# Optimization experiments

Hardware: AMD Instinct MI355X
Metric: run time of the kernel (lower is better)

The kernel has to match this reference:

```python
import jax, jax.numpy as jnp
import numpy as np

N_NODES = 100000
N_EDGES = 3200000
D_FEAT = 128
N_CLASSES = 8


def setup_inputs() -> dict:
    key = jax.random.key(0)
    ks = jax.random.split(key, 8)
    x = jax.random.normal(ks[0], (N_NODES, D_FEAT), dtype=jnp.float32)
    edge_index = jax.random.randint(ks[1], (2, N_EDGES), 0, N_NODES, dtype=jnp.int64)
    W1 = jax.random.normal(ks[2], (D_FEAT, 32), dtype=jnp.float32) / np.sqrt(D_FEAT)
    b1 = jnp.zeros((32,), dtype=jnp.float32)
    W2 = jax.random.normal(ks[3], (32, 16), dtype=jnp.float32) / np.sqrt(32)
    b2 = jnp.zeros((16,), dtype=jnp.float32)
    Wc = jax.random.normal(ks[4], (16, N_CLASSES), dtype=jnp.float32) / np.sqrt(16)
    bc = jnp.zeros((N_CLASSES,), dtype=jnp.float32)
    return {"x": x, "edge_index": edge_index, "W1": W1, "b1": b1,
            "W2": W2, "b2": b2, "Wc": Wc, "bc": bc}


def _gcn_conv(h, src, dst, norm, W, b, num_nodes):
    # PyG GCNConv: linear transform, then sym-normalized scatter-add, then bias
    h = h @ W                                   # [N, out]
    msg = h[src] * norm[:, None]                # [E+N, out] gather + scale
    out = jax.ops.segment_sum(msg, dst, num_segments=num_nodes)
    return out + b


def reference(x, edge_index, W1, b1, W2, b2, Wc, bc):
    num_nodes = x.shape[0]
    loop = jnp.arange(num_nodes, dtype=edge_index.dtype)
    src = jnp.concatenate([edge_index[0], loop])  # add self-loops (PyG default)
    dst = jnp.concatenate([edge_index[1], loop])
    deg = jax.ops.segment_sum(jnp.ones_like(dst, dtype=x.dtype), dst,
                              num_segments=num_nodes)
    dinv = jnp.where(deg > 0, jax.lax.rsqrt(deg), 0.0)
    norm = dinv[src] * dinv[dst]                # symmetric normalization per edge

    h = _gcn_conv(x, src, dst, norm, W1, b1, num_nodes)
    h = jax.nn.relu(h)
    # dropout p=0.5 is identity in eval mode (training=False)
    h = _gcn_conv(h, src, dst, norm, W2, b2, num_nodes)
    h = jax.nn.relu(h)
    logits = h @ Wc + bc
    return jax.nn.log_softmax(logits, axis=1)
```

## Files before the change

### kernel.cpp

```cpp
#include <hip/hip_runtime.h>
#include <math.h>

#define N_NODES 100000
#define N_EDGES 3200000
#define D_FEAT 128
#define H1 32
#define H2 16
#define NC 8

#define NBUCK 391
#define BCAP 12288
#define HCAP 6144
#define EPB 4096
#define EPT 8

#define P_NODES 32
#define P_CAP 3072

typedef short s16x8 __attribute__((ext_vector_type(8)));
typedef float f32x4 __attribute__((ext_vector_type(4)));

__device__ inline unsigned short f2bf(float f) {
    unsigned int u = __float_as_uint(f);
    u += 0x7FFF + ((u >> 16) & 1);
    return (unsigned short)(u >> 16);
}
__device__ inline float bf2f(unsigned short h) {
    return __uint_as_float((unsigned int)h << 16);
}

__device__ inline int wave_scan_incl(int v, int lane) {
#pragma unroll
    for (int off = 1; off < 64; off <<= 1) {
        const int t = __shfl_up(v, off, 64);
        if (lane >= off) v += t;
    }
    return v;
}


__global__ __launch_bounds__(512) void k_bscatter(const int* __restrict__ ei,
                                                  const float* __restrict__ W1,
                                                  int* __restrict__ bucket_cursor,
                                                  unsigned short* __restrict__ W1f,
                                                  int* __restrict__ ebuf) {
    __shared__ int hist[NBUCK];
    __shared__ int lofs[NBUCK];
    __shared__ int rank[NBUCK];
    __shared__ int gb[NBUCK];
    __shared__ int wsum[8];
    __shared__ int s_is64;
    __shared__ int pay[EPB];
    __shared__ unsigned short pbk[EPB];
    const int tid = threadIdx.x;
    const int lane = tid & 63;
    const int wid = tid >> 6;
    for (int i = tid; i < NBUCK; i += 512) { hist[i] = 0; rank[i] = 0; }
    if (tid < 64) {
        int v = ei[2 * tid + 1];
#pragma unroll
        for (int off = 1; off < 64; off <<= 1) v |= __shfl_xor(v, off, 64);
        if (tid == 0) s_is64 = (v == 0) ? 1 : 0;
    }
    if (blockIdx.x == 0) {
        for (int idx = tid; idx < 2 * 4 * 64 * 8; idx += 512) {
            const int j    = idx & 7;
            const int ln   = (idx >> 3) & 63;
            const int kk   = (idx >> 9) & 3;
            const int nt   = idx >> 11;
            const int k = kk * 32 + ((ln >> 4) << 3) + j;
            const int n = nt * 16 + (ln & 15);
            W1f[idx] = f2bf(W1[k * H1 + n]);
        }
    }
    __syncthreads();
    const int e0 = blockIdx.x * EPB;
    const int n = min(EPB, N_EDGES - e0);
    const bool is64 = (s_is64 != 0);
    int rs[EPT], rd[EPT];
    if (is64) {
#pragma unroll
        for (int k = 0; k < EPT / 2; ++k) {
            const int i = 2 * (tid + k * 512);
            if (i < n) {
                const int e = e0 + i;
                const int4 s = *(const int4*)&ei[2 * e];
                const int4 d = *(const int4*)&ei[2 * N_EDGES + 2 * e];
                rs[2 * k] = s.x; rs[2 * k + 1] = s.z;
                rd[2 * k] = d.x; rd[2 * k + 1] = d.z;
                atomicAdd(&hist[d.x >> 8], 1);
                atomicAdd(&hist[d.z >> 8], 1);
            }
        }
    } else {
#pragma unroll
        for (int k = 0; k < EPT / 2; ++k) {
            const int i = 2 * (tid + k * 512);
            if (i < n) {
                const int e = e0 + i;
                const int2 s = *(const int2*)&ei[e];
                const int2 d = *(const int2*)&ei[N_EDGES + e];
                rs[2 * k] = s.x; rs[2 * k + 1] = s.y;
                rd[2 * k] = d.x; rd[2 * k + 1] = d.y;
                atomicAdd(&hist[d.x >> 8], 1);
                atomicAdd(&hist[d.y >> 8], 1);
            }
        }
    }
    __syncthreads();
    const int own = (tid < NBUCK) ? hist[tid] : 0;
    int incl = wave_scan_incl(own, lane);
    if (lane == 63) wsum[wid] = incl;
    __syncthreads();
    if (tid == 0) {
        int r = 0;
#pragma unroll
        for (int w = 0; w < 8; ++w) { const int t = wsum[w]; wsum[w] = r; r += t; }
    }
    __syncthreads();
    incl += wsum[wid];
    if (tid < NBUCK) {
        lofs[tid] = incl - own;
        if (own > 0) gb[tid] = tid * BCAP + atomicAdd(&bucket_cursor[tid], own);
    }
    __syncthreads();
#pragma unroll
    for (int k = 0; k < EPT / 2; ++k) {
        const int i = 2 * (tid + k * 512);
        if (i < n) {
#pragma unroll
            for (int j = 0; j < 2; ++j) {
                const int b = rd[2 * k + j] >> 8;
                const int p = lofs[b] + atomicAdd(&rank[b], 1);
                pay[p] = (rs[2 * k + j] << 8) | (rd[2 * k + j] & 255);
                pbk[p] = (unsigned short)b;
            }
        }
    }
    __syncthreads();
    for (int p = tid; p < n; p += 512) {
        const int b = pbk[p];
        ebuf[gb[b] + (p - lofs[b])] = pay[p];
    }
}


__global__ __launch_bounds__(512) void k_deg(const int* __restrict__ ebuf,
                                             const int* __restrict__ bucket_cursor,
                                             float* __restrict__ dinv) {
    __shared__ int cnt[256];
    const int b = blockIdx.x;
    const int tid = threadIdx.x;
    if (tid < 256) cnt[tid] = 0;
    __syncthreads();
    const int nb = bucket_cursor[b];
    const int rb = b * BCAP;
    for (int i = tid; i < nb; i += 512)
        atomicAdd(&cnt[ebuf[rb + i] & 255], 1);
    __syncthreads();
    if (tid < 256) {
        const int v = (b << 8) + tid;
        if (v < N_NODES) dinv[v] = rsqrtf(1.0f + (float)cnt[tid]);
    }
}


__global__ __launch_bounds__(256) void k_gemm1m(const float* __restrict__ x,
                                                const unsigned short* __restrict__ W1f,
                                                const float* __restrict__ dinv,
                                                unsigned int* __restrict__ u1q) {
    __shared__ float os[4][16][33];
    const int tid = threadIdx.x;
    const int w = tid >> 6;
    const int lane = tid & 63;
    const int row0 = (blockIdx.x * 4 + w) * 16;
    const bool act = (row0 < N_NODES);
    if (act) {
        const int m = lane & 15;
        const int quad = lane >> 4;
        const s16x8* bf = (const s16x8*)W1f;
        f32x4 acc0 = {0.f, 0.f, 0.f, 0.f};
        f32x4 acc1 = {0.f, 0.f, 0.f, 0.f};
#pragma unroll
        for (int kk = 0; kk < 4; ++kk) {
            const float* xp = x + (size_t)(row0 + m) * D_FEAT + kk * 32 + quad * 8;
            const float4 p0 = ((const float4*)xp)[0];
            const float4 p1 = ((const float4*)xp)[1];
            s16x8 a;
            a[0] = (short)f2bf(p0.x); a[1] = (short)f2bf(p0.y);
            a[2] = (short)f2bf(p0.z); a[3] = (short)f2bf(p0.w);
            a[4] = (short)f2bf(p1.x); a[5] = (short)f2bf(p1.y);
            a[6] = (short)f2bf(p1.z); a[7] = (short)f2bf(p1.w);
            acc0 = __builtin_amdgcn_mfma_f32_16x16x32_bf16(a, bf[kk * 64 + lane], acc0, 0, 0, 0);
            acc1 = __builtin_amdgcn_mfma_f32_16x16x32_bf16(a, bf[(4 + kk) * 64 + lane], acc1, 0, 0, 0);
        }
#pragma unroll
        for (int r = 0; r < 4; ++r) {
            os[w][quad * 4 + r][m]      = acc0[r];
            os[w][quad * 4 + r][16 + m] = acc1[r];
        }
    }
    __syncthreads();
    if (act) {
        const int rl = lane >> 2;
        const int seg = lane & 3;
        const int row = row0 + rl;
        const float dv = dinv[row];
        const float* p = &os[w][rl][seg * 8];
        unsigned int pk0 = __builtin_amdgcn_cvt_pk_fp8_f32(p[0] * dv, p[1] * dv, 0u, false);
        pk0 = __builtin_amdgcn_cvt_pk_fp8_f32(p[2] * dv, p[3] * dv, pk0, true);
        unsigned int pk1 = __builtin_amdgcn_cvt_pk_fp8_f32(p[4] * dv, p[5] * dv, 0u, false);
        pk1 = __builtin_amdgcn_cvt_pk_fp8_f32(p[6] * dv, p[7] * dv, pk1, true);
        uint2 o; o.x = pk0; o.y = pk1;
        ((uint2*)u1q)[(size_t)row * 4 + seg] = o;
    }
}


#define ACC8(Q) do { \
    a0 += __builtin_amdgcn_cvt_f32_fp8((Q).x, 0); \
    a1 += __builtin_amdgcn_cvt_f32_fp8((Q).x, 1); \
    a2 += __builtin_amdgcn_cvt_f32_fp8((Q).x, 2); \
    a3 += __builtin_amdgcn_cvt_f32_fp8((Q).x, 3); \
    a4 += __builtin_amdgcn_cvt_f32_fp8((Q).y, 0); \
    a5 += __builtin_amdgcn_cvt_f32_fp8((Q).y, 1); \
    a6 += __builtin_amdgcn_cvt_f32_fp8((Q).y, 2); \
    a7 += __builtin_amdgcn_cvt_f32_fp8((Q).y, 3); \
} while (0)

__global__ __launch_bounds__(512) void k_fuse1(const int* __restrict__ ebuf,
                                               const int* __restrict__ bucket_cursor,
                                               const unsigned int* __restrict__ u1q,
                                               const float* __restrict__ b1,
                                               const float* __restrict__ W2,
                                               int* __restrict__ row_ptr,
                                               int* __restrict__ col_idx,
                                               unsigned int* __restrict__ u2b) {
    __shared__ int srt[HCAP];
    __shared__ int cnt[256];
    __shared__ int cur[256];
    __shared__ int wsum[8];
    __shared__ int wsum2[4];
    __shared__ float Ws[H1 * H2];
    __shared__ float hs[128][33];
    __shared__ int s_wb, s_base, s_nh;
    const int b = blockIdx.x >> 1;
    const int h = blockIdx.x & 1;
    const int tid = threadIdx.x;
    const int lane = tid & 63;
    const int wid = tid >> 6;
    if (tid < 256) cnt[tid] = 0;
    for (int i = tid; i < H1 * H2; i += 512) Ws[i] = W2[i];
    const int own0 = (tid < NBUCK) ? bucket_cursor[tid] : 0;
    int incl0 = wave_scan_incl(own0, lane);
    if (lane == 63) wsum[wid] = incl0;
    __syncthreads();
    if (tid == 0) {
        int r = 0;
#pragma unroll
        for (int w = 0; w < 8; ++w) { const int t = wsum[w]; wsum[w] = r; r += t; }
    }
    __syncthreads();
    if (tid == b) s_wb = incl0 + wsum[wid] - own0;
    const int nb = bucket_cursor[b];
    const int rb = b * BCAP;
    for (int i = tid; i < nb; i += 512)
        atomicAdd(&cnt[ebuf[rb + i] & 255], 1);
    __syncthreads();
    int ownc = 0, inclc = 0;
    if (tid < 256) {
        ownc = cnt[tid];
        inclc = wave_scan_incl(ownc, lane);
        if (lane == 63) wsum2[wid] = inclc;
    }
    __syncthreads();
    if (tid == 0) {
        int r = 0;
#pragma unroll
        for (int w = 0; w < 4; ++w) { const int t = wsum2[w]; wsum2[w] = r; r += t; }
    }
    __syncthreads();
    const int wb = s_wb;
    if (tid < 256) {
        inclc += wsum2[wid];
        const int excl = inclc - ownc;
        cur[tid] = excl;
        const int v = (b << 8) + tid;
        if (v <= N_NODES) row_ptr[v] = wb + excl;
    }
    __syncthreads();
    if (tid == 0) {
        s_base = cur[h * 128];
        s_nh = (h ? nb : cur[128]) - cur[h * 128];
    }
    __syncthreads();
    const int base_h = s_base;
    const int nh = s_nh;
    for (int i = tid; i < nb; i += 512) {
        const int pk = ebuf[rb + i];
        const int dl = pk & 255;
        if ((dl >> 7) == h) {
            const int slot = atomicAdd(&cur[dl], 1);
            srt[slot - base_h] = pk >> 8;
        }
    }
    __syncthreads();
    for (int i = tid; i < nh; i += 512)
        col_idx[wb + base_h + i] = srt[i];
    const int nnl = tid >> 2;
    const int lq = tid & 3;
    const int nn = h * 128 + nnl;
    const int v = (b << 8) + nn;
    if (v < N_NODES) {
        const uint2* base = (const uint2*)u1q;
        const uint2 q = base[(size_t)v * 4 + lq];
        float a0 = __builtin_amdgcn_cvt_f32_fp8(q.x, 0);
        float a1 = __builtin_amdgcn_cvt_f32_fp8(q.x, 1);
        float a2 = __builtin_amdgcn_cvt_f32_fp8(q.x, 2);
        float a3 = __builtin_amdgcn_cvt_f32_fp8(q.x, 3);
        float a4 = __builtin_amdgcn_cvt_f32_fp8(q.y, 0);
        float a5 = __builtin_amdgcn_cvt_f32_fp8(q.y, 1);
        float a6 = __builtin_amdgcn_cvt_f32_fp8(q.y, 2);
        float a7 = __builtin_amdgcn_cvt_f32_fp8(q.y, 3);
        const int cn = cnt[nn];
        const int e = cur[nn] - base_h;
        int j = e - cn;
        for (; j + 7 < e; j += 8) {
            const int s0 = srt[j + 0];
            const int s1 = srt[j + 1];
            const int s2 = srt[j + 2];
            const int s3 = srt[j + 3];
            const int s4 = srt[j + 4];
            const int s5 = srt[j + 5];
            const int s6 = srt[j + 6];
            const int s7 = srt[j + 7];
            const uint2 q0 = base[(size_t)s0 * 4 + lq];
            const uint2 q1 = base[(size_t)s1 * 4 + lq];
            const uint2 q2 = base[(size_t)s2 * 4 + lq];
            const uint2 q3 = base[(size_t)s3 * 4 + lq];
            const uint2 q4 = base[(size_t)s4 * 4 + lq];
            const uint2 q5 = base[(size_t)s5 * 4 + lq];
            const uint2 q6 = base[(size_t)s6 * 4 + lq];
            const uint2 q7 = base[(size_t)s7 * 4 + lq];
            ACC8(q0); ACC8(q1); ACC8(q2); ACC8(q3);
            ACC8(q4); ACC8(q5); ACC8(q6); ACC8(q7);
        }
        for (; j + 3 < e; j += 4) {
            const int s0 = srt[j + 0];
            const int s1 = srt[j + 1];
            const int s2 = srt[j + 2];
            const int s3 = srt[j + 3];
            const uint2 q0 = base[(size_t)s0 * 4 + lq];
            const uint2 q1 = base[(size_t)s1 * 4 + lq];
            const uint2 q2 = base[(size_t)s2 * 4 + lq];
            const uint2 q3 = base[(size_t)s3 * 4 + lq];
            ACC8(q0); ACC8(q1); ACC8(q2); ACC8(q3);
        }
        for (; j < e; ++j) {
            const uint2 qq = base[(size_t)srt[j] * 4 + lq];
            ACC8(qq);
        }
        const float dv = rsqrtf(1.0f + (float)cn);
        const float4 bb0 = ((const float4*)b1)[lq * 2];
        const float4 bb1 = ((const float4*)b1)[lq * 2 + 1];
        float* hp = &hs[nnl][lq * 8];
        hp[0] = fmaxf(fmaf(a0, dv, bb0.x), 0.0f);
        hp[1] = fmaxf(fmaf(a1, dv, bb0.y), 0.0f);
        hp[2] = fmaxf(fmaf(a2, dv, bb0.z), 0.0f);
        hp[3] = fmaxf(fmaf(a3, dv, bb0.w), 0.0f);
        hp[4] = fmaxf(fmaf(a4, dv, bb1.x), 0.0f);
        hp[5] = fmaxf(fmaf(a5, dv, bb1.y), 0.0f);
        hp[6] = fmaxf(fmaf(a6, dv, bb1.z), 0.0f);
        hp[7] = fmaxf(fmaf(a7, dv, bb1.w), 0.0f);
        if (lq == 0) hs[nnl][32] = dv;
    }
    __syncthreads();
    {
        const int nn2 = tid >> 2;
        const int jq = tid & 3;
        const int v2 = (b << 8) + h * 128 + nn2;
        if (v2 < N_NODES) {
            const int j0 = jq * 4;
            const float dv = hs[nn2][32];
            float s0 = 0.f, s1 = 0.f, s2 = 0.f, s3 = 0.f;
#pragma unroll
            for (int k = 0; k < H1; ++k) {
                const float hk = hs[nn2][k];
                s0 = fmaf(hk, Ws[k * H2 + j0 + 0], s0);
                s1 = fmaf(hk, Ws[k * H2 + j0 + 1], s1);
                s2 = fmaf(hk, Ws[k * H2 + j0 + 2], s2);
                s3 = fmaf(hk, Ws[k * H2 + j0 + 3], s3);
            }
            uint2 o;
            o.x = (unsigned int)f2bf(s0 * dv) | ((unsigned int)f2bf(s1 * dv) << 16);
            o.y = (unsigned int)f2bf(s2 * dv) | ((unsigned int)f2bf(s3 * dv) << 16);
            ((uint2*)u2b)[(size_t)v2 * 4 + jq] = o;
        }
    }
}


#define ACC4(Q) do { \
    a0 += bf2f((unsigned short)(Q).x); \
    a1 += bf2f((unsigned short)((Q).x >> 16)); \
    a2 += bf2f((unsigned short)(Q).y); \
    a3 += bf2f((unsigned short)((Q).y >> 16)); \
} while (0)

__global__ __launch_bounds__(256) void k_pull2f(const int* __restrict__ row_ptr,
                                                const int* __restrict__ col_idx,
                                                const float* __restrict__ dinv,
                                                const unsigned int* __restrict__ u2b,
                                                const float* __restrict__ b2,
                                                const float* __restrict__ Wc,
                                                const float* __restrict__ bc,
                                                float* __restrict__ out) {
    __shared__ float hs[P_NODES][17];
    __shared__ float Wcs[H2 * NC];
    __shared__ float bcs[NC];
    __shared__ int lidx[P_CAP];
    const int tid = threadIdx.x;
    if (tid < H2 * NC) Wcs[tid] = Wc[tid];
    if (tid < NC) bcs[tid] = bc[tid];
    const int v0 = blockIdx.x * P_NODES;
    const int base_off = row_ptr[v0];
    const int range = row_ptr[v0 + P_NODES] - base_off;
    const bool ovf = (range > P_CAP);
    const int stg = ovf ? 0 : range;
    for (int j = tid; j < stg; j += 256) lidx[j] = col_idx[base_off + j];
    __syncthreads();
    const int n = tid >> 3;
    const int half = (tid >> 2) & 1;
    const int lq = tid & 3;
    const int v = v0 + n;
    const uint2* base = (const uint2*)u2b;
    float a0 = 0.f, a1 = 0.f, a2 = 0.f, a3 = 0.f;
    if (half == 0) {
        const uint2 q = base[(size_t)v * 4 + lq];
        a0 = bf2f((unsigned short)q.x); a1 = bf2f((unsigned short)(q.x >> 16));
        a2 = bf2f((unsigned short)q.y); a3 = bf2f((unsigned short)(q.y >> 16));
    }
    const int beg = row_ptr[v] - base_off;
    const int end = row_ptr[v + 1] - base_off;
    int i = beg + half;
    if (!ovf) {
        for (; i + 14 < end; i += 16) {
            const int s0 = lidx[i];
            const int s1 = lidx[i + 2];
            const int s2 = lidx[i + 4];
            const int s3 = lidx[i + 6];
            const int s4 = lidx[i + 8];
            const int s5 = lidx[i + 10];
            const int s6 = lidx[i + 12];
            const int s7 = lidx[i + 14];
            const uint2 q0 = base[(size_t)s0 * 4 + lq];
            const uint2 q1 = base[(size_t)s1 * 4 + lq];
            const uint2 q2 = base[(size_t)s2 * 4 + lq];
            const uint2 q3 = base[(size_t)s3 * 4 + lq];
            const uint2 q4 = base[(size_t)s4 * 4 + lq];
            const uint2 q5 = base[(size_t)s5 * 4 + lq];
            const uint2 q6 = base[(size_t)s6 * 4 + lq];
            const uint2 q7 = base[(size_t)s7 * 4 + lq];
            ACC4(q0); ACC4(q1); ACC4(q2); ACC4(q3);
            ACC4(q4); ACC4(q5); ACC4(q6); ACC4(q7);
        }
        for (; i + 6 < end; i += 8) {
            const int s0 = lidx[i];
            const int s1 = lidx[i + 2];
            const int s2 = lidx[i + 4];
            const int s3 = lidx[i + 6];
            const uint2 q0 = base[(size_t)s0 * 4 + lq];
            const uint2 q1 = base[(size_t)s1 * 4 + lq];
            const uint2 q2 = base[(size_t)s2 * 4 + lq];
            const uint2 q3 = base[(size_t)s3 * 4 + lq];
            ACC4(q0); ACC4(q1); ACC4(q2); ACC4(q3);
        }
        for (; i < end; i += 2) {
            const uint2 qq = base[(size_t)lidx[i] * 4 + lq];
            ACC4(qq);
        }
    } else {
        const int* gp = col_idx + base_off;
        for (; i + 14 < end; i += 16) {
            const int s0 = gp[i];
            const int s1 = gp[i + 2];
            const int s2 = gp[i + 4];
            const int s3 = gp[i + 6];
            const int s4 = gp[i + 8];
            const int s5 = gp[i + 10];
            const int s6 = gp[i + 12];
            const int s7 = gp[i + 14];
            const uint2 q0 = base[(size_t)s0 * 4 + lq];
            const uint2 q1 = base[(size_t)s1 * 4 + lq];
            const uint2 q2 = base[(size_t)s2 * 4 + lq];
            const uint2 q3 = base[(size_t)s3 * 4 + lq];
            const uint2 q4 = base[(size_t)s4 * 4 + lq];
            const uint2 q5 = base[(size_t)s5 * 4 + lq];
            const uint2 q6 = base[(size_t)s6 * 4 + lq];
            const uint2 q7 = base[(size_t)s7 * 4 + lq];
            ACC4(q0); ACC4(q1); ACC4(q2); ACC4(q3);
            ACC4(q4); ACC4(q5); ACC4(q6); ACC4(q7);
        }
        for (; i < end; i += 2) {
            const uint2 qq = base[(size_t)gp[i] * 4 + lq];
            ACC4(qq);
        }
    }
    a0 += __shfl_xor(a0, 4, 64); a1 += __shfl_xor(a1, 4, 64);
    a2 += __shfl_xor(a2, 4, 64); a3 += __shfl_xor(a3, 4, 64);
    if (half == 0) {
        const float dv = dinv[v];
        const float4 bb = ((const float4*)b2)[lq];
        float* hp = &hs[n][lq * 4];
        hp[0] = fmaxf(fmaf(a0, dv, bb.x), 0.0f);
        hp[1] = fmaxf(fmaf(a1, dv, bb.y), 0.0f);
        hp[2] = fmaxf(fmaf(a2, dv, bb.z), 0.0f);
        hp[3] = fmaxf(fmaf(a3, dv, bb.w), 0.0f);
    }
    __syncthreads();
    if (tid < P_NODES) {
        const int vv = v0 + tid;
        float lg[NC];
#pragma unroll
        for (int j = 0; j < NC; ++j) lg[j] = bcs[j];
#pragma unroll
        for (int k = 0; k < H2; ++k) {
            const float hk = hs[tid][k];
#pragma unroll
            for (int j = 0; j < NC; ++j)
                lg[j] = fmaf(hk, Wcs[k * NC + j], lg[j]);
        }
        float m = lg[0];
#pragma unroll
        for (int j = 1; j < NC; ++j) m = fmaxf(m, lg[j]);
        float s = 0.0f;
#pragma unroll
        for (int j = 0; j < NC; ++j) s += expf(lg[j] - m);
        const float lse = logf(s) + m;
        float4 o0, o1;
        o0.x = lg[0] - lse; o0.y = lg[1] - lse;
        o0.z = lg[2] - lse; o0.w = lg[3] - lse;
        o1.x = lg[4] - lse; o1.y = lg[5] - lse;
        o1.z = lg[6] - lse; o1.w = lg[7] - lse;
        float4* op = (float4*)(out + (size_t)vv * NC);
        op[0] = o0; op[1] = o1;
    }
}


extern "C" void kernel_launch(void* const* d_in, const int* in_sizes, int n_in,
                              void* d_out, int out_size, void* d_ws, size_t ws_size,
                              hipStream_t stream) {
    const float* x   = (const float*)d_in[0];
    const int*   ei  = (const int*)d_in[1];
    const float* W1  = (const float*)d_in[2];
    const float* b1  = (const float*)d_in[3];
    const float* W2  = (const float*)d_in[4];
    const float* b2  = (const float*)d_in[5];
    const float* Wc  = (const float*)d_in[6];
    const float* bc  = (const float*)d_in[7];
    float* out = (float*)d_out;

    int*   bucket_cursor = (int*)d_ws;
    float* dinv          = (float*)(bucket_cursor + 512);
    unsigned short* W1f  = (unsigned short*)((int*)dinv + 100000);
    int*   row_ptr       = (int*)W1f + 2048;
    int*   col_idx       = row_ptr + 100016;
    unsigned int* u1q    = (unsigned int*)(col_idx + 3200000);
    unsigned int* u2b    = u1q + 800000;
    int*   ebuf          = (int*)(u2b + 800000);

    hipMemsetAsync(bucket_cursor, 0, 512 * sizeof(int), stream);
    k_bscatter<<<(N_EDGES + EPB - 1) / EPB, 512, 0, stream>>>(ei, W1, bucket_cursor, W1f, ebuf);
    k_deg   <<<NBUCK, 512, 0, stream>>>(ebuf, bucket_cursor, dinv);
    k_gemm1m<<<(N_NODES + 63) / 64, 256, 0, stream>>>(x, W1f, dinv, u1q);
    k_fuse1 <<<NBUCK * 2, 512, 0, stream>>>(ebuf, bucket_cursor, u1q, b1, W2, row_ptr, col_idx, u2b);
    k_pull2f<<<N_NODES / P_NODES, 256, 0, stream>>>(row_ptr, col_idx, dinv, u2b, b2, Wc, bc, out);
}
```

Measured before the change: 205.3 us.

## Fuse degree count into first GEMM kernel and reuse counts in fuse1

Merges the degree-counting kernel with the first-layer MFMA GEMM so each 256-node bucket block computes in-degrees and then the projected, dinv-scaled FP8 features for those same nodes. The per-node counts go to a new degc buffer, and fuse1 loads them instead of re-histogramming the bucket's edges with shared atomics. This saves one launch and one pass over ebuf. In exchange the GEMM now runs on only 391 blocks of 512 threads, each wave doing two 16-row tiles, so it has less parallelism than the previous ~1563-block launch.

```diff
diff --git a/kernel.cpp b/kernel.cpp
--- a/kernel.cpp
+++ b/kernel.cpp
@@ -145,9 +145,14 @@
 }
 
 
-__global__ __launch_bounds__(512) void k_deg(const int* __restrict__ ebuf,
-                                             const int* __restrict__ bucket_cursor,
-                                             float* __restrict__ dinv) {
+__global__ __launch_bounds__(512) void k_gemm1d(const float* __restrict__ x,
+                                                const unsigned short* __restrict__ W1f,
+                                                const int* __restrict__ ebuf,
+                                                const int* __restrict__ bucket_cursor,
+                                                int* __restrict__ degc,
+                                                float* __restrict__ dinv,
+                                                unsigned int* __restrict__ u1q) {
+    __shared__ float os[8][2][16][33];
     __shared__ int cnt[256];
     const int b = blockIdx.x;
     const int tid = threadIdx.x;
@@ -160,30 +165,25 @@
     __syncthreads();
     if (tid < 256) {
         const int v = (b << 8) + tid;
+        degc[v] = cnt[tid];
         if (v < N_NODES) dinv[v] = rsqrtf(1.0f + (float)cnt[tid]);
     }
-}
-
-
-__global__ __launch_bounds__(256) void k_gemm1m(const float* __restrict__ x,
-                                                const unsigned short* __restrict__ W1f,
-                                                const float* __restrict__ dinv,
-                                                unsigned int* __restrict__ u1q) {
-    __shared__ float os[4][16][33];
-    const int tid = threadIdx.x;
     const int w = tid >> 6;
     const int lane = tid & 63;
-    const int row0 = (blockIdx.x * 4 + w) * 16;
-    const bool act = (row0 < N_NODES);
-    if (act) {
-        const int m = lane & 15;
-        const int quad = lane >> 4;
-        const s16x8* bf = (const s16x8*)W1f;
+    const int m = lane & 15;
+    const int quad = lane >> 4;
+    const s16x8* bf = (const s16x8*)W1f;
+    const int tA = w * 2, tB = w * 2 + 1;
+    const int rowA = (b << 8) + tA * 16;
+    const int rowB = (b << 8) + tB * 16;
+    const bool actA = (rowA < N_NODES);
+    const bool actB = (rowB < N_NODES);
+    if (actA) {
         f32x4 acc0 = {0.f, 0.f, 0.f, 0.f};
         f32x4 acc1 = {0.f, 0.f, 0.f, 0.f};
 #pragma unroll
         for (int kk = 0; kk < 4; ++kk) {
-            const float* xp = x + (size_t)(row0 + m) * D_FEAT + kk * 32 + quad * 8;
+            const float* xp = x + (size_t)(rowA + m) * D_FEAT + kk * 32 + quad * 8;
             const float4 p0 = ((const float4*)xp)[0];
             const float4 p1 = ((const float4*)xp)[1];
             s16x8 a;
@@ -196,17 +196,50 @@
         }
 #pragma unroll
         for (int r = 0; r < 4; ++r) {
-            os[w][quad * 4 + r][m]      = acc0[r];
-            os[w][quad * 4 + r][16 + m] = acc1[r];
-        }
-    }
-    __syncthreads();
-    if (act) {
-        const int rl = lane >> 2;
-        const int seg = lane & 3;
-        const int row = row0 + rl;
-        const float dv = dinv[row];
-        const float* p = &os[w][rl][seg * 8];
+            os[w][0][quad * 4 + r][m]      = acc0[r];
+            os[w][0][quad * 4 + r][16 + m] = acc1[r];
+        }
+    }
+    if (actB) {
+        f32x4 acc0 = {0.f, 0.f, 0.f, 0.f};
+        f32x4 acc1 = {0.f, 0.f, 0.f, 0.f};
+#pragma unroll
+        for (int kk = 0; kk < 4; ++kk) {
+            const float* xp = x + (size_t)(rowB + m) * D_FEAT + kk * 32 + quad * 8;
+            const float4 p0 = ((const float4*)xp)[0];
+            const float4 p1 = ((const float4*)xp)[1];
+            s16x8 a;
+            a[0] = (short)f2bf(p0.x); a[1] = (short)f2bf(p0.y);
+            a[2] = (short)f2bf(p0.z); a[3] = (short)f2bf(p0.w);
+            a[4] = (short)f2bf(p1.x); a[5] = (short)f2bf(p1.y);
+            a[6] = (short)f2bf(p1.z); a[7] = (short)f2bf(p1.w);
+            acc0 = __builtin_amdgcn_mfma_f32_16x16x32_bf16(a, bf[kk * 64 + lane], acc0, 0, 0, 0);
+            acc1 = __builtin_amdgcn_mfma_f32_16x16x32_bf16(a, bf[(4 + kk) * 64 + lane], acc1, 0, 0, 0);
+        }
+#pragma unroll
+        for (int r = 0; r < 4; ++r) {
+            os[w][1][quad * 4 + r][m]      = acc0[r];
+            os[w][1][quad * 4 + r][16 + m] = acc1[r];
+        }
+    }
+    __syncthreads();
+    const int rl = lane >> 2;
+    const int seg = lane & 3;
+    if (actA) {
+        const int row = rowA + rl;
+        const float dv = rsqrtf(1.0f + (float)cnt[tA * 16 + rl]);
+        const float* p = &os[w][0][rl][seg * 8];
+        unsigned int pk0 = __builtin_amdgcn_cvt_pk_fp8_f32(p[0] * dv, p[1] * dv, 0u, false);
+        pk0 = __builtin_amdgcn_cvt_pk_fp8_f32(p[2] * dv, p[3] * dv, pk0, true);
+        unsigned int pk1 = __builtin_amdgcn_cvt_pk_fp8_f32(p[4] * dv, p[5] * dv, 0u, false);
+        pk1 = __builtin_amdgcn_cvt_pk_fp8_f32(p[6] * dv, p[7] * dv, pk1, true);
+        uint2 o; o.x = pk0; o.y = pk1;
+        ((uint2*)u1q)[(size_t)row * 4 + seg] = o;
+    }
+    if (actB) {
+        const int row = rowB + rl;
+        const float dv = rsqrtf(1.0f + (float)cnt[tB * 16 + rl]);
+        const float* p = &os[w][1][rl][seg * 8];
         unsigned int pk0 = __builtin_amdgcn_cvt_pk_fp8_f32(p[0] * dv, p[1] * dv, 0u, false);
         pk0 = __builtin_amdgcn_cvt_pk_fp8_f32(p[2] * dv, p[3] * dv, pk0, true);
         unsigned int pk1 = __builtin_amdgcn_cvt_pk_fp8_f32(p[4] * dv, p[5] * dv, 0u, false);
@@ -230,6 +263,7 @@
 
 __global__ __launch_bounds__(512) void k_fuse1(const int* __restrict__ ebuf,
                                                const int* __restrict__ bucket_cursor,
+                                               const int* __restrict__ degc,
                                                const unsigned int* __restrict__ u1q,
                                                const float* __restrict__ b1,
                                                const float* __restrict__ W2,
@@ -249,7 +283,7 @@
     const int tid = threadIdx.x;
     const int lane = tid & 63;
     const int wid = tid >> 6;
-    if (tid < 256) cnt[tid] = 0;
+    if (tid < 256) cnt[tid] = degc[(b << 8) + tid];
     for (int i = tid; i < H1 * H2; i += 512) Ws[i] = W2[i];
     const int own0 = (tid < NBUCK) ? bucket_cursor[tid] : 0;
     int incl0 = wave_scan_incl(own0, lane);
@@ -264,9 +298,6 @@
     if (tid == b) s_wb = incl0 + wsum[wid] - own0;
     const int nb = bucket_cursor[b];
     const int rb = b * BCAP;
-    for (int i = tid; i < nb; i += 512)
-        atomicAdd(&cnt[ebuf[rb + i] & 255], 1);
-    __syncthreads();
     int ownc = 0, inclc = 0;
     if (tid < 256) {
         ownc = cnt[tid];
@@ -563,7 +594,8 @@
 
     int*   bucket_cursor = (int*)d_ws;
     float* dinv          = (float*)(bucket_cursor + 512);
-    unsigned short* W1f  = (unsigned short*)((int*)dinv + 100000);
+    int*   degc          = (int*)dinv + 100000;
+    unsigned short* W1f  = (unsigned short*)(degc + 100096);
     int*   row_ptr       = (int*)W1f + 2048;
     int*   col_idx       = row_ptr + 100016;
     unsigned int* u1q    = (unsigned int*)(col_idx + 3200000);
@@ -572,8 +604,7 @@
 
     hipMemsetAsync(bucket_cursor, 0, 512 * sizeof(int), stream);
     k_bscatter<<<(N_EDGES + EPB - 1) / EPB, 512, 0, stream>>>(ei, W1, bucket_cursor, W1f, ebuf);
-    k_deg   <<<NBUCK, 512, 0, stream>>>(ebuf, bucket_cursor, dinv);
-    k_gemm1m<<<(N_NODES + 63) / 64, 256, 0, stream>>>(x, W1f, dinv, u1q);
-    k_fuse1 <<<NBUCK * 2, 512, 0, stream>>>(ebuf, bucket_cursor, u1q, b1, W2, row_ptr, col_idx, u2b);
+    k_gemm1d<<<NBUCK, 512, 0, stream>>>(x, W1f, ebuf, bucket_cursor, degc, dinv, u1q);
+    k_fuse1 <<<NBUCK * 2, 512, 0, stream>>>(ebuf, bucket_cursor, degc, u1q, b1, W2, row_ptr, col_idx, u2b);
     k_pull2f<<<N_NODES / P_NODES, 256, 0, stream>>>(row_ptr, col_idx, dinv, u2b, b2, Wc, bc, out);
 }
```

Result: no change. 203.7 us (-0.8%).

## Merge GEMM1 into bucket-scatter launch and reuse degree counts in fuse1

Applied to the files above, without the earlier changes.

The x@W1 MFMA GEMM now runs in extra blocks of the edge bucket-scatter kernel, so the dense GEMM overlaps the scatter instead of waiting for degrees. It writes unscaled bf16 results to a temporary buffer that aliases col_idx. The degree kernel then applies dinv and quantizes to fp8, and saves per-node counts so fuse1 no longer re-histograms the edge buckets. This removes one launch and one full edge pass, at the cost of an extra bf16 round-trip through memory and a second rounding step (bf16, then fp8).

```diff
diff --git a/kernel.cpp b/kernel.cpp
--- a/kernel.cpp
+++ b/kernel.cpp
@@ -13,6 +13,7 @@
 #define HCAP 6144
 #define EPB 4096
 #define EPT 8
+#define NSB ((N_EDGES + EPB - 1) / EPB)
 
 #define P_NODES 32
 #define P_CAP 3072
@@ -39,44 +40,98 @@
 }
 
 
-__global__ __launch_bounds__(512) void k_bscatter(const int* __restrict__ ei,
-                                                  const float* __restrict__ W1,
-                                                  int* __restrict__ bucket_cursor,
-                                                  unsigned short* __restrict__ W1f,
-                                                  int* __restrict__ ebuf) {
-    __shared__ int hist[NBUCK];
-    __shared__ int lofs[NBUCK];
-    __shared__ int rank[NBUCK];
-    __shared__ int gb[NBUCK];
-    __shared__ int wsum[8];
-    __shared__ int s_is64;
-    __shared__ int pay[EPB];
-    __shared__ unsigned short pbk[EPB];
+__global__ __launch_bounds__(512) void k_pre(const int* __restrict__ ei,
+                                             const float* __restrict__ x,
+                                             const float* __restrict__ W1,
+                                             int* __restrict__ bucket_cursor,
+                                             int* __restrict__ ebuf,
+                                             unsigned short* __restrict__ y16) {
+    __shared__ union {
+        struct {
+            int hist[NBUCK], lofs[NBUCK], rank[NBUCK], gb[NBUCK], wsum[8], is64;
+            int pay[EPB];
+            unsigned short pbk[EPB];
+        } sc;
+        struct {
+            unsigned short wf[2 * 4 * 64 * 8];
+            float os[8][16][33];
+        } gm;
+    } u;
     const int tid = threadIdx.x;
     const int lane = tid & 63;
     const int wid = tid >> 6;
-    for (int i = tid; i < NBUCK; i += 512) { hist[i] = 0; rank[i] = 0; }
+
+    if (blockIdx.x >= NSB) {
+        const int gb_ = blockIdx.x - NSB;
+        for (int idx = tid; idx < 2 * 4 * 64 * 8; idx += 512) {
+            const int j  = idx & 7;
+            const int ln = (idx >> 3) & 63;
+            const int kk = (idx >> 9) & 3;
+            const int nt = idx >> 11;
+            const int k = kk * 32 + ((ln >> 4) << 3) + j;
+            const int n = nt * 16 + (ln & 15);
+            u.gm.wf[idx] = f2bf(W1[k * H1 + n]);
+        }
+        __syncthreads();
+        const int w = tid >> 6;
+        const int m = lane & 15;
+        const int quad = lane >> 4;
+        const int rl = lane >> 2;
+        const int seg = lane & 3;
+        const s16x8* bf = (const s16x8*)u.gm.wf;
+#pragma unroll
+        for (int t = 0; t < 2; ++t) {
+            const int row0 = (gb_ << 8) + (w * 2 + t) * 16;
+            const bool act = (row0 < N_NODES);
+            if (act) {
+                f32x4 acc0 = {0.f, 0.f, 0.f, 0.f};
+                f32x4 acc1 = {0.f, 0.f, 0.f, 0.f};
+#pragma unroll
+                for (int kk = 0; kk < 4; ++kk) {
+                    const float* xp = x + (size_t)(row0 + m) * D_FEAT + kk * 32 + quad * 8;
+                    const float4 p0 = ((const float4*)xp)[0];
+                    const float4 p1 = ((const float4*)xp)[1];
+                    s16x8 a;
+                    a[0] = (short)f2bf(p0.x); a[1] = (short)f2bf(p0.y);
+                    a[2] = (short)f2bf(p0.z); a[3] = (short)f2bf(p0.w);
+                    a[4] = (short)f2bf(p1.x); a[5] = (short)f2bf(p1.y);
+                    a[6] = (short)f2bf(p1.z); a[7] = (short)f2bf(p1.w);
+                    acc0 = __builtin_amdgcn_mfma_f32_16x16x32_bf16(a, bf[kk * 64 + lane], acc0, 0, 0, 0);
+                    acc1 = __builtin_amdgcn_mfma_f32_16x16x32_bf16(a, bf[(4 + kk) * 64 + lane], acc1, 0, 0, 0);
+                }
+#pragma unroll
+                for (int r = 0; r < 4; ++r) {
+                    u.gm.os[w][quad * 4 + r][m]      = acc0[r];
+                    u.gm.os[w][quad * 4 + r][16 + m] = acc1[r];
+                }
+            }
+            __syncthreads();
+            if (act) {
+                const int row = row0 + rl;
+                const float* p = &u.gm.os[w][rl][seg * 8];
+                uint4 o;
+                o.x = (unsigned int)f2bf(p[0]) | ((unsigned int)f2bf(p[1]) << 16);
+                o.y = (unsigned int)f2bf(p[2]) | ((unsigned int)f2bf(p[3]) << 16);
+                o.z = (unsigned int)f2bf(p[4]) | ((unsigned int)f2bf(p[5]) << 16);
+                o.w = (unsigned int)f2bf(p[6]) | ((unsigned int)f2bf(p[7]) << 16);
+                *(uint4*)(y16 + (size_t)row * 32 + seg * 8) = o;
+            }
+            __syncthreads();
+        }
+        return;
+    }
+
+    for (int i = tid; i < NBUCK; i += 512) { u.sc.hist[i] = 0; u.sc.rank[i] = 0; }
     if (tid < 64) {
         int v = ei[2 * tid + 1];
 #pragma unroll
         for (int off = 1; off < 64; off <<= 1) v |= __shfl_xor(v, off, 64);
-        if (tid == 0) s_is64 = (v == 0) ? 1 : 0;
-    }
-    if (blockIdx.x == 0) {
-        for (int idx = tid; idx < 2 * 4 * 64 * 8; idx += 512) {
-            const int j    = idx & 7;
-            const int ln   = (idx >> 3) & 63;
-            const int kk   = (idx >> 9) & 3;
-            const int nt   = idx >> 11;
-            const int k = kk * 32 + ((ln >> 4) << 3) + j;
-            const int n = nt * 16 + (ln & 15);
-            W1f[idx] = f2bf(W1[k * H1 + n]);
-        }
+        if (tid == 0) u.sc.is64 = (v == 0) ? 1 : 0;
     }
     __syncthreads();
     const int e0 = blockIdx.x * EPB;
     const int n = min(EPB, N_EDGES - e0);
-    const bool is64 = (s_is64 != 0);
+    const bool is64 = (u.sc.is64 != 0);
     int rs[EPT], rd[EPT];
     if (is64) {
 #pragma unroll
@@ -88,8 +143,8 @@
                 const int4 d = *(const int4*)&ei[2 * N_EDGES + 2 * e];
                 rs[2 * k] = s.x; rs[2 * k + 1] = s.z;
                 rd[2 * k] = d.x; rd[2 * k + 1] = d.z;
-                atomicAdd(&hist[d.x >> 8], 1);
-                atomicAdd(&hist[d.z >> 8], 1);
+                atomicAdd(&u.sc.hist[d.x >> 8], 1);
+                atomicAdd(&u.sc.hist[d.z >> 8], 1);
             }
         }
     } else {
@@ -102,26 +157,26 @@
                 const int2 d = *(const int2*)&ei[N_EDGES + e];
                 rs[2 * k] = s.x; rs[2 * k + 1] = s.y;
                 rd[2 * k] = d.x; rd[2 * k + 1] = d.y;
-                atomicAdd(&hist[d.x >> 8], 1);
-                atomicAdd(&hist[d.y >> 8], 1);
+                atomicAdd(&u.sc.hist[d.x >> 8], 1);
+                atomicAdd(&u.sc.hist[d.y >> 8], 1);
             }
         }
     }
     __syncthreads();
-    const int own = (tid < NBUCK) ? hist[tid] : 0;
+    const int own = (tid < NBUCK) ? u.sc.hist[tid] : 0;
     int incl = wave_scan_incl(own, lane);
-    if (lane == 63) wsum[wid] = incl;
+    if (lane == 63) u.sc.wsum[wid] = incl;
     __syncthreads();
     if (tid == 0) {
         int r = 0;
 #pragma unroll
-        for (int w = 0; w < 8; ++w) { const int t = wsum[w]; wsum[w] = r; r += t; }
-    }
-    __syncthreads();
-    incl += wsum[wid];
+        for (int w = 0; w < 8; ++w) { const int t = u.sc.wsum[w]; u.sc.wsum[w] = r; r += t; }
+    }
+    __syncthreads();
+    incl += u.sc.wsum[wid];
     if (tid < NBUCK) {
-        lofs[tid] = incl - own;
-        if (own > 0) gb[tid] = tid * BCAP + atomicAdd(&bucket_cursor[tid], own);
+        u.sc.lofs[tid] = incl - own;
+        if (own > 0) u.sc.gb[tid] = tid * BCAP + atomicAdd(&bucket_cursor[tid], own);
     }
     __syncthreads();
 #pragma unroll
@@ -131,23 +186,26 @@
 #pragma unroll
             for (int j = 0; j < 2; ++j) {
                 const int b = rd[2 * k + j] >> 8;
-                const int p = lofs[b] + atomicAdd(&rank[b], 1);
-                pay[p] = (rs[2 * k + j] << 8) | (rd[2 * k + j] & 255);
-                pbk[p] = (unsigned short)b;
+                const int p = u.sc.lofs[b] + atomicAdd(&u.sc.rank[b], 1);
+                u.sc.pay[p] = (rs[2 * k + j] << 8) | (rd[2 * k + j] & 255);
+                u.sc.pbk[p] = (unsigned short)b;
             }
         }
     }
     __syncthreads();
     for (int p = tid; p < n; p += 512) {
-        const int b = pbk[p];
-        ebuf[gb[b] + (p - lofs[b])] = pay[p];
-    }
-}
-
-
-__global__ __launch_bounds__(512) void k_deg(const int* __restrict__ ebuf,
+        const int b = u.sc.pbk[p];
+        ebuf[u.sc.gb[b] + (p - u.sc.lofs[b])] = u.sc.pay[p];
+    }
+}
+
+
+__global__ __launch_bounds__(512) void k_mid(const int* __restrict__ ebuf,
                                              const int* __restrict__ bucket_cursor,
-                                             float* __restrict__ dinv) {
+                                             const unsigned short* __restrict__ y16,
+                                             int* __restrict__ degc,
+                                             float* __restrict__ dinv,
+                                             unsigned int* __restrict__ u1q) {
     __shared__ int cnt[256];
     const int b = blockIdx.x;
     const int tid = threadIdx.x;
@@ -160,59 +218,32 @@
     __syncthreads();
     if (tid < 256) {
         const int v = (b << 8) + tid;
-        if (v < N_NODES) dinv[v] = rsqrtf(1.0f + (float)cnt[tid]);
-    }
-}
-
-
-__global__ __launch_bounds__(256) void k_gemm1m(const float* __restrict__ x,
-                                                const unsigned short* __restrict__ W1f,
-                                                const float* __restrict__ dinv,
-                                                unsigned int* __restrict__ u1q) {
-    __shared__ float os[4][16][33];
-    const int tid = threadIdx.x;
-    const int w = tid >> 6;
-    const int lane = tid & 63;
-    const int row0 = (blockIdx.x * 4 + w) * 16;
-    const bool act = (row0 < N_NODES);
-    if (act) {
-        const int m = lane & 15;
-        const int quad = lane >> 4;
-        const s16x8* bf = (const s16x8*)W1f;
-        f32x4 acc0 = {0.f, 0.f, 0.f, 0.f};
-        f32x4 acc1 = {0.f, 0.f, 0.f, 0.f};
-#pragma unroll
-        for (int kk = 0; kk < 4; ++kk) {
-            const float* xp = x + (size_t)(row0 + m) * D_FEAT + kk * 32 + quad * 8;
-            const float4 p0 = ((const float4*)xp)[0];
-            const float4 p1 = ((const float4*)xp)[1];
-            s16x8 a;
-            a[0] = (short)f2bf(p0.x); a[1] = (short)f2bf(p0.y);
-            a[2] = (short)f2bf(p0.z); a[3] = (short)f2bf(p0.w);
-            a[4] = (short)f2bf(p1.x); a[5] = (short)f2bf(p1.y);
-            a[6] = (short)f2bf(p1.z); a[7] = (short)f2bf(p1.w);
-            acc0 = __builtin_amdgcn_mfma_f32_16x16x32_bf16(a, bf[kk * 64 + lane], acc0, 0, 0, 0);
-            acc1 = __builtin_amdgcn_mfma_f32_16x16x32_bf16(a, bf[(4 + kk) * 64 + lane], acc1, 0, 0, 0);
-        }
-#pragma unroll
-        for (int r = 0; r < 4; ++r) {
-            os[w][quad * 4 + r][m]      = acc0[r];
-            os[w][quad * 4 + r][16 + m] = acc1[r];
-        }
-    }
-    __syncthreads();
-    if (act) {
-        const int rl = lane >> 2;
-        const int seg = lane & 3;
-        const int row = row0 + rl;
-        const float dv = dinv[row];
-        const float* p = &os[w][rl][seg * 8];
-        unsigned int pk0 = __builtin_amdgcn_cvt_pk_fp8_f32(p[0] * dv, p[1] * dv, 0u, false);
-        pk0 = __builtin_amdgcn_cvt_pk_fp8_f32(p[2] * dv, p[3] * dv, pk0, true);
-        unsigned int pk1 = __builtin_amdgcn_cvt_pk_fp8_f32(p[4] * dv, p[5] * dv, 0u, false);
-        pk1 = __builtin_amdgcn_cvt_pk_fp8_f32(p[6] * dv, p[7] * dv, pk1, true);
-        uint2 o; o.x = pk0; o.y = pk1;
-        ((uint2*)u1q)[(size_t)row * 4 + seg] = o;
+        const int cn = cnt[tid];
+        degc[v] = cn;
+        if (v < N_NODES) {
+            const float dv = rsqrtf(1.0f + (float)cn);
+            dinv[v] = dv;
+            unsigned int r[16];
+            const uint4* yp = (const uint4*)(y16 + (size_t)v * 32);
+            *(uint4*)&r[0]  = yp[0];
+            *(uint4*)&r[4]  = yp[1];
+            *(uint4*)&r[8]  = yp[2];
+            *(uint4*)&r[12] = yp[3];
+            unsigned int wq[8];
+#pragma unroll
+            for (int j = 0; j < 8; ++j) {
+                const float c0 = bf2f((unsigned short)r[2 * j]) * dv;
+                const float c1 = bf2f((unsigned short)(r[2 * j] >> 16)) * dv;
+                const float c2 = bf2f((unsigned short)r[2 * j + 1]) * dv;
+                const float c3 = bf2f((unsigned short)(r[2 * j + 1] >> 16)) * dv;
+                unsigned int pk = __builtin_amdgcn_cvt_pk_fp8_f32(c0, c1, 0u, false);
+                wq[j] = __builtin_amdgcn_cvt_pk_fp8_f32(c2, c3, pk, true);
+            }
+            uint4 oa; oa.x = wq[0]; oa.y = wq[1]; oa.z = wq[2]; oa.w = wq[3];
+            uint4 ob; ob.x = wq[4]; ob.y = wq[5]; ob.z = wq[6]; ob.w = wq[7];
+            ((uint4*)u1q)[(size_t)v * 2]     = oa;
+            ((uint4*)u1q)[(size_t)v * 2 + 1] = ob;
+        }
     }
 }
 
@@ -230,6 +261,7 @@
 
 __global__ __launch_bounds__(512) void k_fuse1(const int* __restrict__ ebuf,
                                                const int* __restrict__ bucket_cursor,
+                                               const int* __restrict__ degc,
                                                const unsigned int* __restrict__ u1q,
                                                const float* __restrict__ b1,
                                                const float* __restrict__ W2,
@@ -249,7 +281,7 @@
     const int tid = threadIdx.x;
     const int lane = tid & 63;
     const int wid = tid >> 6;
-    if (tid < 256) cnt[tid] = 0;
+    if (tid < 256) cnt[tid] = degc[(b << 8) + tid];
     for (int i = tid; i < H1 * H2; i += 512) Ws[i] = W2[i];
     const int own0 = (tid < NBUCK) ? bucket_cursor[tid] : 0;
     int incl0 = wave_scan_incl(own0, lane);
@@ -264,9 +296,6 @@
     if (tid == b) s_wb = incl0 + wsum[wid] - own0;
     const int nb = bucket_cursor[b];
     const int rb = b * BCAP;
-    for (int i = tid; i < nb; i += 512)
-        atomicAdd(&cnt[ebuf[rb + i] & 255], 1);
-    __syncthreads();
     int ownc = 0, inclc = 0;
     if (tid < 256) {
         ownc = cnt[tid];
@@ -563,17 +592,17 @@
 
     int*   bucket_cursor = (int*)d_ws;
     float* dinv          = (float*)(bucket_cursor + 512);
-    unsigned short* W1f  = (unsigned short*)((int*)dinv + 100000);
-    int*   row_ptr       = (int*)W1f + 2048;
+    int*   degc          = (int*)dinv + 100000;
+    int*   row_ptr       = degc + 100096;
     int*   col_idx       = row_ptr + 100016;
     unsigned int* u1q    = (unsigned int*)(col_idx + 3200000);
     unsigned int* u2b    = u1q + 800000;
     int*   ebuf          = (int*)(u2b + 800000);
+    unsigned short* y16  = (unsigned short*)col_idx;
 
     hipMemsetAsync(bucket_cursor, 0, 512 * sizeof(int), stream);
-    k_bscatter<<<(N_EDGES + EPB - 1) / EPB, 512, 0, stream>>>(ei, W1, bucket_cursor, W1f, ebuf);
-    k_deg   <<<NBUCK, 512, 0, stream>>>(ebuf, bucket_cursor, dinv);
-    k_gemm1m<<<(N_NODES + 63) / 64, 256, 0, stream>>>(x, W1f, dinv, u1q);
-    k_fuse1 <<<NBUCK * 2, 512, 0, stream>>>(ebuf, bucket_cursor, u1q, b1, W2, row_ptr, col_idx, u2b);
+    k_pre <<<NSB + NBUCK, 512, 0, stream>>>(ei, x, W1, bucket_cursor, ebuf, y16);
+    k_mid <<<NBUCK, 512, 0, stream>>>(ebuf, bucket_cursor, y16, degc, dinv, u1q);
+    k_fuse1<<<NBUCK * 2, 512, 0, stream>>>(ebuf, bucket_cursor, degc, u1q, b1, W2, row_ptr, col_idx, u2b);
     k_pull2f<<<N_NODES / P_NODES, 256, 0, stream>>>(row_ptr, col_idx, dinv, u2b, b2, Wc, bc, out);
 }
```

Result: no change. 201.9 us (-1.6%).
